# Performance work log

Measured on AMD Instinct MI355X. Metric: run time of the kernel, lower is better.

## Reference

```python
import jax, jax.numpy as jnp
import numpy as np

N, T, D, H = 64, 512, 512, 512


def setup_inputs() -> dict:
    key = jax.random.key(0)
    k1, k2, k3, k4 = jax.random.split(key, 4)
    x = jax.random.normal(k1, (N, T, D), dtype=jnp.float32)
    h0 = jax.random.normal(k2, (N, H), dtype=jnp.float32)
    Wx = jax.random.normal(k3, (D, H), dtype=jnp.float32) / jnp.sqrt(jnp.float32(D))
    Wh = jax.random.normal(k4, (H, H), dtype=jnp.float32) / jnp.sqrt(jnp.float32(H))
    b = jnp.zeros((H,), dtype=jnp.float32)
    return {"x": x, "h0": h0, "Wx": Wx, "Wh": Wh, "b": b}


def reference(x, h0, Wx, Wh, b):
    # Precompute the input-to-hidden projection for all timesteps at once
    # (one big GEMM), then scan the sequential hidden-state recurrence.
    xWx = jnp.einsum('ntd,dh->nth', x, Wx) + b  # (N, T, H)

    def step(h_prev, xw_t):
        h_next = jnp.tanh(xw_t + h_prev @ Wh)  # (N, H)
        return h_next, h_next

    # scan over time: move T to leading axis
    _, h_seq = jax.lax.scan(step, h0, jnp.swapaxes(xWx, 0, 1))  # (T, N, H)
    return jnp.swapaxes(h_seq, 0, 1)  # (N, T, H)
```

## Files before the change

### kernel.cpp

```cpp
#include <hip/hip_runtime.h>
#include <hip/hip_bf16.h>
#include <cmath>


#define DH     512
#define NSEQ   64
#define TSTEPS 512
#define MTOT   32768

__global__ __launch_bounds__(256) void xw_gemm(
    const float* __restrict__ X,
    const float* __restrict__ Wx,
    const float* __restrict__ b,
    float* __restrict__ XW)
{
    __shared__ float As[16][64];
    __shared__ float Bs[16][64];

    const int bm = blockIdx.x * 64;
    const int bn = blockIdx.y * 64;
    const int tid = threadIdx.x;
    const int tr = tid >> 4;
    const int tc = tid & 15;

    float acc[4][4] = {};

    for (int k0 = 0; k0 < DH; k0 += 16) {
        {
            int m  = tid >> 2;
            int kk = (tid & 3) * 4;
            const float4 v = *(const float4*)&X[(size_t)(bm + m) * DH + k0 + kk];
            As[kk + 0][m] = v.x; As[kk + 1][m] = v.y;
            As[kk + 2][m] = v.z; As[kk + 3][m] = v.w;
        }
        {
            int k  = tid >> 4;
            int j4 = (tid & 15) * 4;
            *(float4*)&Bs[k][j4] = *(const float4*)&Wx[(size_t)(k0 + k) * DH + bn + j4];
        }
        __syncthreads();

        #pragma unroll
        for (int k = 0; k < 16; ++k) {
            float a0 = As[k][tr * 4 + 0], a1 = As[k][tr * 4 + 1];
            float a2 = As[k][tr * 4 + 2], a3 = As[k][tr * 4 + 3];
            float b0 = Bs[k][tc * 4 + 0], b1 = Bs[k][tc * 4 + 1];
            float b2 = Bs[k][tc * 4 + 2], b3 = Bs[k][tc * 4 + 3];
            acc[0][0] += a0 * b0; acc[0][1] += a0 * b1; acc[0][2] += a0 * b2; acc[0][3] += a0 * b3;
            acc[1][0] += a1 * b0; acc[1][1] += a1 * b1; acc[1][2] += a1 * b2; acc[1][3] += a1 * b3;
            acc[2][0] += a2 * b0; acc[2][1] += a2 * b1; acc[2][2] += a2 * b2; acc[2][3] += a2 * b3;
            acc[3][0] += a3 * b0; acc[3][1] += a3 * b1; acc[3][2] += a3 * b2; acc[3][3] += a3 * b3;
        }
        __syncthreads();
    }

    #pragma unroll
    for (int i = 0; i < 4; ++i) {
        const size_t row = (size_t)(bm + tr * 4 + i);
        #pragma unroll
        for (int j = 0; j < 4; ++j) {
            const int col = bn + tc * 4 + j;
            XW[row * DH + col] = acc[i][j] + b[col];
        }
    }
}

__global__ __launch_bounds__(512, 2) void rnn_rec4c(
    const float* __restrict__ Wh,
    const float* __restrict__ h0,
    float* __restrict__ out,
    unsigned long long* __restrict__ hbuf)
{
    __shared__ float hsh[DH];
    __shared__ float partb[8][DH / 4];

    const int bid  = blockIdx.x;
    const int xcd  = bid & 7;
    const int idx  = bid >> 3;
    const int seq  = xcd * 8 + (idx & 7);
    const int part = idx >> 3;
    const int tid  = threadIdx.x;
    const int cp   = tid & 63;
    const int s    = tid >> 6;
    const int colbase = part * 128;
    const int c0   = colbase + cp * 2;

    float2 wv[64];
    #pragma unroll
    for (int k = 0; k < 64; ++k)
        wv[k] = *(const float2*)&Wh[(size_t)(s * 64 + k) * DH + c0];
    #pragma unroll
    for (int k = 0; k < 64; ++k)
        asm volatile("" : "+v"(wv[k].x), "+v"(wv[k].y));

    if (tid < DH) hsh[tid] = h0[(size_t)seq * DH + tid];
    __syncthreads();

    float* __restrict__ outn = out + (size_t)seq * TSTEPS * DH;
    const int mycol = colbase + tid;
    float xw_cur = (tid < 128) ? outn[mycol] : 0.0f;

    const int r = tid - 128;
    const int rcol = (r < colbase) ? r : (r + 128);

    for (int t = 0; t < TSTEPS; ++t) {
        float xw_next = 0.0f;
        if (tid < 128 && t < TSTEPS - 1)
            xw_next = outn[(size_t)(t + 1) * DH + mycol];

        float a0 = 0.0f, a1 = 0.0f;
        #pragma unroll
        for (int q = 0; q < 16; ++q) {
            const float4 h4 = *(const float4*)&hsh[s * 64 + q * 4];
            a0 += h4.x * wv[4 * q + 0].x; a1 += h4.x * wv[4 * q + 0].y;
            a0 += h4.y * wv[4 * q + 1].x; a1 += h4.y * wv[4 * q + 1].y;
            a0 += h4.z * wv[4 * q + 2].x; a1 += h4.z * wv[4 * q + 2].y;
            a0 += h4.w * wv[4 * q + 3].x; a1 += h4.w * wv[4 * q + 3].y;
        }
        partb[s][cp * 2 + 0] = a0;
        partb[s][cp * 2 + 1] = a1;
        __syncthreads();

        unsigned long long* hb = &hbuf[((size_t)(t & 1) * NSEQ + seq) * DH];

        if (tid < 128) {
            float ssum = partb[0][tid] + partb[1][tid] + partb[2][tid] + partb[3][tid]
                       + partb[4][tid] + partb[5][tid] + partb[6][tid] + partb[7][tid];
            const float hval = tanhf(xw_cur + ssum);
            hsh[mycol] = hval;
            if (t < TSTEPS - 1) {
                const unsigned long long v =
                    ((unsigned long long)(unsigned)(t + 1) << 32) |
                    (unsigned long long)__float_as_uint(hval);
                __hip_atomic_store(&hb[mycol], v,
                                   __ATOMIC_RELAXED, __HIP_MEMORY_SCOPE_AGENT);
            }
            outn[(size_t)t * DH + mycol] = hval;
            xw_cur = xw_next;
        } else if (t < TSTEPS - 1) {
            unsigned long long v;
            do {
                v = __hip_atomic_load(&hb[rcol], __ATOMIC_RELAXED,
                                      __HIP_MEMORY_SCOPE_AGENT);
            } while ((unsigned)(v >> 32) < (unsigned)(t + 1));
            hsh[rcol] = __uint_as_float((unsigned)v);
        }
        __syncthreads();
    }
}

__global__ __launch_bounds__(1024) void rnn_rec(
    const float* __restrict__ Wh,
    const float* __restrict__ h0,
    float* __restrict__ out)
{
    __shared__ float hsh[DH];
    __shared__ float part[8][DH];

    const int n     = blockIdx.x;
    const int tid   = threadIdx.x;
    const int jgrp  = tid & 127;
    const int ks    = tid >> 7;
    const int kbase = ks * 64;

    if (tid < DH) hsh[tid] = h0[(size_t)n * DH + tid];
    __syncthreads();

    const float4* __restrict__ Wh4 = (const float4*)Wh;
    float* __restrict__ outn = out + (size_t)n * TSTEPS * DH;

    float xw_cur = (tid < DH) ? outn[tid] : 0.0f;

    for (int t = 0; t < TSTEPS; ++t) {
        float xw_next = 0.0f;
        if (tid < DH && t < TSTEPS - 1) xw_next = outn[(size_t)(t + 1) * DH + tid];

        float4 acc = {0.0f, 0.0f, 0.0f, 0.0f};
        #pragma unroll 8
        for (int k = 0; k < 64; ++k) {
            const float hk = hsh[kbase + k];
            const float4 w = Wh4[(size_t)(kbase + k) * 128 + jgrp];
            acc.x += hk * w.x; acc.y += hk * w.y;
            acc.z += hk * w.z; acc.w += hk * w.w;
        }
        *(float4*)&part[ks][jgrp * 4] = acc;
        __syncthreads();

        if (tid < DH) {
            const int j = tid;
            float sum = part[0][j] + part[1][j] + part[2][j] + part[3][j]
                      + part[4][j] + part[5][j] + part[6][j] + part[7][j];
            const float hv = tanhf(xw_cur + sum);
            hsh[j] = hv;
            outn[(size_t)t * DH + j] = hv;
            xw_cur = xw_next;
        }
        __syncthreads();
    }
}

extern "C" void kernel_launch(void* const* d_in, const int* in_sizes, int n_in,
                              void* d_out, int out_size, void* d_ws, size_t ws_size,
                              hipStream_t stream) {
    const float* x  = (const float*)d_in[0];
    const float* h0 = (const float*)d_in[1];
    const float* Wx = (const float*)d_in[2];
    const float* Wh = (const float*)d_in[3];
    const float* b  = (const float*)d_in[4];
    float* out = (float*)d_out;

    xw_gemm<<<dim3(MTOT / 64, DH / 64), 256, 0, stream>>>(x, Wx, b, out);

    const size_t hbuf_bytes = (size_t)2 * NSEQ * DH * sizeof(unsigned long long);
    if (ws_size >= hbuf_bytes) {
        unsigned long long* hbuf = (unsigned long long*)d_ws;
        hipMemsetAsync(hbuf, 0, hbuf_bytes, stream);
        rnn_rec4c<<<256, 512, 0, stream>>>(Wh, h0, out, hbuf);
    } else {
        rnn_rec<<<NSEQ, 1024, 0, stream>>>(Wh, h0, out);
    }
}
```

Measured before the change: 927.8 us.

## Give each wave its own h slice to drop the second per-step barrier

The recurrent kernel now gives each wave its own 64-entry slice of the hidden state. A wave fills that slice either by reducing its own columns or by polling the global flag buffer, so only that wave ever reads it. Because of this, the second __syncthreads per timestep is removed, and the partial-sum buffer is double-buffered so the next step's writes cannot clash with this step's reads. The inner dot product now uses packed two-wide FMA, and the next xW value is loaded after the tanh instead of being prefetched. The intent is to shorten the serial critical path of each timestep. The cost is that the next xW load is no longer prefetched, and correctness now depends on careful reasoning about wave-local ordering.

Measured after the change: 890.8 us. 4.0% less time.

```diff
diff --git a/kernel.cpp b/kernel.cpp
--- a/kernel.cpp
+++ b/kernel.cpp
@@ -7,6 +7,8 @@
 #define NSEQ   64
 #define TSTEPS 512
 #define MTOT   32768
+
+typedef float v2f __attribute__((ext_vector_type(2)));
 
 __global__ __launch_bounds__(256) void xw_gemm(
     const float* __restrict__ X,
@@ -65,14 +67,14 @@
     }
 }
 
-__global__ __launch_bounds__(512, 2) void rnn_rec4c(
+__global__ __launch_bounds__(512, 2) void rnn_rec5(
     const float* __restrict__ Wh,
     const float* __restrict__ h0,
     float* __restrict__ out,
     unsigned long long* __restrict__ hbuf)
 {
-    __shared__ float hsh[DH];
-    __shared__ float partb[8][DH / 4];
+    __shared__ float hslice[8][64];
+    __shared__ float partb[2][8][128];
 
     const int bid  = blockIdx.x;
     const int xcd  = bid & 7;
@@ -80,72 +82,72 @@
     const int seq  = xcd * 8 + (idx & 7);
     const int part = idx >> 3;
     const int tid  = threadIdx.x;
-    const int cp   = tid & 63;
+    const int lane = tid & 63;
     const int s    = tid >> 6;
     const int colbase = part * 128;
-    const int c0   = colbase + cp * 2;
-
-    float2 wv[64];
+    const int c0   = colbase + lane * 2;
+
+    v2f wv[64];
     #pragma unroll
     for (int k = 0; k < 64; ++k)
-        wv[k] = *(const float2*)&Wh[(size_t)(s * 64 + k) * DH + c0];
+        wv[k] = *(const v2f*)&Wh[(size_t)(s * 64 + k) * DH + c0];
     #pragma unroll
     for (int k = 0; k < 64; ++k)
-        asm volatile("" : "+v"(wv[k].x), "+v"(wv[k].y));
-
-    if (tid < DH) hsh[tid] = h0[(size_t)seq * DH + tid];
-    __syncthreads();
+        asm volatile("" : "+v"(wv[k]));
+
+    const int rwave = s - 2 * part;
+    const bool is_reducer = (rwave == 0) | (rwave == 1);
+    const int q     = rwave * 64 + lane;
+    const int mycol = colbase + q;
+    const int slot  = s * 64 + lane;
+
+    hslice[s][lane] = h0[(size_t)seq * DH + slot];
 
     float* __restrict__ outn = out + (size_t)seq * TSTEPS * DH;
-    const int mycol = colbase + tid;
-    float xw_cur = (tid < 128) ? outn[mycol] : 0.0f;
-
-    const int r = tid - 128;
-    const int rcol = (r < colbase) ? r : (r + 128);
+    float xw_cur = is_reducer ? outn[mycol] : 0.0f;
 
     for (int t = 0; t < TSTEPS; ++t) {
-        float xw_next = 0.0f;
-        if (tid < 128 && t < TSTEPS - 1)
-            xw_next = outn[(size_t)(t + 1) * DH + mycol];
-
-        float a0 = 0.0f, a1 = 0.0f;
+        const int buf = t & 1;
+
+        v2f acc = {0.0f, 0.0f};
         #pragma unroll
-        for (int q = 0; q < 16; ++q) {
-            const float4 h4 = *(const float4*)&hsh[s * 64 + q * 4];
-            a0 += h4.x * wv[4 * q + 0].x; a1 += h4.x * wv[4 * q + 0].y;
-            a0 += h4.y * wv[4 * q + 1].x; a1 += h4.y * wv[4 * q + 1].y;
-            a0 += h4.z * wv[4 * q + 2].x; a1 += h4.z * wv[4 * q + 2].y;
-            a0 += h4.w * wv[4 * q + 3].x; a1 += h4.w * wv[4 * q + 3].y;
-        }
-        partb[s][cp * 2 + 0] = a0;
-        partb[s][cp * 2 + 1] = a1;
-        __syncthreads();
-
-        unsigned long long* hb = &hbuf[((size_t)(t & 1) * NSEQ + seq) * DH];
-
-        if (tid < 128) {
-            float ssum = partb[0][tid] + partb[1][tid] + partb[2][tid] + partb[3][tid]
-                       + partb[4][tid] + partb[5][tid] + partb[6][tid] + partb[7][tid];
+        for (int qq = 0; qq < 16; ++qq) {
+            const float4 h4 = *(const float4*)&hslice[s][qq * 4];
+            v2f hb;
+            hb.x = h4.x; hb.y = h4.x; acc = __builtin_elementwise_fma(hb, wv[4*qq+0], acc);
+            hb.x = h4.y; hb.y = h4.y; acc = __builtin_elementwise_fma(hb, wv[4*qq+1], acc);
+            hb.x = h4.z; hb.y = h4.z; acc = __builtin_elementwise_fma(hb, wv[4*qq+2], acc);
+            hb.x = h4.w; hb.y = h4.w; acc = __builtin_elementwise_fma(hb, wv[4*qq+3], acc);
+        }
+        *(v2f*)&partb[buf][s][lane * 2] = acc;
+        __syncthreads();
+
+        unsigned long long* hb64 = &hbuf[((size_t)buf * NSEQ + seq) * DH];
+        if (is_reducer) {
+            float ssum = partb[buf][0][q] + partb[buf][1][q]
+                       + partb[buf][2][q] + partb[buf][3][q]
+                       + partb[buf][4][q] + partb[buf][5][q]
+                       + partb[buf][6][q] + partb[buf][7][q];
             const float hval = tanhf(xw_cur + ssum);
-            hsh[mycol] = hval;
             if (t < TSTEPS - 1) {
                 const unsigned long long v =
                     ((unsigned long long)(unsigned)(t + 1) << 32) |
                     (unsigned long long)__float_as_uint(hval);
-                __hip_atomic_store(&hb[mycol], v,
+                __hip_atomic_store(&hb64[mycol], v,
                                    __ATOMIC_RELAXED, __HIP_MEMORY_SCOPE_AGENT);
             }
+            hslice[s][lane] = hval;
             outn[(size_t)t * DH + mycol] = hval;
-            xw_cur = xw_next;
+            if (t < TSTEPS - 1)
+                xw_cur = outn[(size_t)(t + 1) * DH + mycol];
         } else if (t < TSTEPS - 1) {
             unsigned long long v;
             do {
-                v = __hip_atomic_load(&hb[rcol], __ATOMIC_RELAXED,
+                v = __hip_atomic_load(&hb64[slot], __ATOMIC_RELAXED,
                                       __HIP_MEMORY_SCOPE_AGENT);
             } while ((unsigned)(v >> 32) < (unsigned)(t + 1));
-            hsh[rcol] = __uint_as_float((unsigned)v);
-        }
-        __syncthreads();
+            hslice[s][lane] = __uint_as_float((unsigned)v);
+        }
     }
 }
 
@@ -215,7 +217,7 @@
     if (ws_size >= hbuf_bytes) {
         unsigned long long* hbuf = (unsigned long long*)d_ws;
         hipMemsetAsync(hbuf, 0, hbuf_bytes, stream);
-        rnn_rec4c<<<256, 512, 0, stream>>>(Wh, h0, out, hbuf);
+        rnn_rec5<<<256, 512, 0, stream>>>(Wh, h0, out, hbuf);
     } else {
         rnn_rec<<<NSEQ, 1024, 0, stream>>>(Wh, h0, out);
     }
```
